# Kernel optimization log

Hardware: AMD Instinct MI355X
Metric: run time of the kernel (lower is better)

Reference implementation:

```python
import jax, jax.numpy as jnp
import numpy as np

HIDDEN = 2048
NUM_HEADS = 16
NUM_KV_HEADS = 8
HEAD_DIM = 128
EPS = 1e-6
ROPE_THETA = 10000.0
T = 2048
Q_SIZE = NUM_HEADS * HEAD_DIM          # 2048
KV_SIZE = NUM_KV_HEADS * HEAD_DIM      # 1024


def setup_inputs() -> dict:
    key = jax.random.key(0)
    k1, k2, k3, k4, k5 = jax.random.split(key, 5)
    positions = jnp.arange(T, dtype=jnp.int32)
    hidden_states = jax.random.normal(k1, (T, HIDDEN), dtype=jnp.float32)
    s = 0.02
    qkv_w = jax.random.normal(k2, (Q_SIZE + 2 * KV_SIZE, HIDDEN), dtype=jnp.float32) * s
    o_w = jax.random.normal(k3, (HIDDEN, Q_SIZE), dtype=jnp.float32) * s
    q_norm_w = jnp.ones((HEAD_DIM,), dtype=jnp.float32) + 0.1 * jax.random.normal(k4, (HEAD_DIM,), dtype=jnp.float32)
    k_norm_w = jnp.ones((HEAD_DIM,), dtype=jnp.float32) + 0.1 * jax.random.normal(k5, (HEAD_DIM,), dtype=jnp.float32)
    return {"positions": positions, "hidden_states": hidden_states,
            "qkv_w": qkv_w, "q_norm_w": q_norm_w, "k_norm_w": k_norm_w, "o_w": o_w}


def _rms_norm(x, w):
    # x: [T, H, D], normalize over last dim
    var = jnp.mean(x * x, axis=-1, keepdims=True)
    return x * jax.lax.rsqrt(var + EPS) * w


def _rope(x, positions):
    # neox-style rotary over full head_dim; x: [T, H, D]
    half = HEAD_DIM // 2
    inv_freq = 1.0 / (ROPE_THETA ** (jnp.arange(0, half, dtype=jnp.float32) / half))
    freqs = positions.astype(jnp.float32)[:, None] * inv_freq  # [T, D/2]
    cos = jnp.cos(freqs)[:, None, :]  # [T, 1, D/2]
    sin = jnp.sin(freqs)[:, None, :]
    x1, x2 = x[..., :half], x[..., half:]
    return jnp.concatenate([x1 * cos - x2 * sin, x2 * cos + x1 * sin], axis=-1)


def reference(positions, hidden_states, qkv_w, q_norm_w, k_norm_w, o_w):
    G = NUM_HEADS // NUM_KV_HEADS  # query groups per kv head
    scale = HEAD_DIM ** -0.5
    qkv = hidden_states @ qkv_w.T  # [T, Q+2KV]
    q, k, v = jnp.split(qkv, [Q_SIZE, Q_SIZE + KV_SIZE], axis=-1)
    q = q.reshape(T, NUM_HEADS, HEAD_DIM)
    k = k.reshape(T, NUM_KV_HEADS, HEAD_DIM)
    v = v.reshape(T, NUM_KV_HEADS, HEAD_DIM)
    # qkv_bias=False path -> per-head RMSNorm on q and k
    q = _rms_norm(q, q_norm_w)
    k = _rms_norm(k, k_norm_w)
    q = _rope(q, positions)
    k = _rope(k, positions)
    # GQA causal attention
    qg = q.reshape(T, NUM_KV_HEADS, G, HEAD_DIM)
    scores = jnp.einsum('qkgd,skd->kgqs', qg, k) * scale  # [KV, G, T, T]
    causal = positions[:, None] >= positions[None, :]  # [T, T]
    scores = jnp.where(causal, scores, jnp.finfo(scores.dtype).min)
    probs = jax.nn.softmax(scores, axis=-1)
    ctx = jnp.einsum('kgqs,skd->qkgd', probs, v)  # [T, KV, G, D]
    ctx = ctx.reshape(T, Q_SIZE)
    return ctx @ o_w.T  # [T, HIDDEN]
```

## Files before the change

### kernel.cpp

```cpp
#include <hip/hip_runtime.h>
#include <math.h>

#define T_SEQ     2048
#define HIDDEN_   2048
#define NUM_HEADS 16
#define NUM_KV    8
#define HEAD_DIM  128
#define Q_SIZE    2048
#define KV_SIZE   1024
#define QKV_N     4096
#define QK_N      3072
#define EPS_      1e-6f

typedef __attribute__((ext_vector_type(8))) short short8;
typedef __attribute__((ext_vector_type(4))) float floatx4;

__device__ __forceinline__ unsigned short f2bf(float f) {
    unsigned int u = __float_as_uint(f);
    u += 0x7fffu + ((u >> 16) & 1u);
    return (unsigned short)(u >> 16);
}
__device__ __forceinline__ float b2f(unsigned short u) {
    return __uint_as_float((unsigned int)u << 16);
}

__device__ __forceinline__ void stage16(const unsigned short* g, unsigned short* lds_base) {
    __builtin_amdgcn_global_load_lds(
        (const __attribute__((address_space(1))) unsigned int*)g,
        (__attribute__((address_space(3))) unsigned int*)lds_base, 16, 0, 0);
}

#define H4 (T_SEQ * HIDDEN_ / 4)
#define W4 (QKV_N * HIDDEN_ / 4)
#define O4 (Q_SIZE * HIDDEN_ / 4)

__global__ __launch_bounds__(256) void convert_all(
    const float* __restrict__ hidden, const float* __restrict__ qkv_w,
    const float* __restrict__ o_w, unsigned short* __restrict__ hbf,
    unsigned short* __restrict__ wbf, unsigned short* __restrict__ obf)
{
    int i = blockIdx.x * 256 + threadIdx.x;
    const float4* src;
    ushort4* dst;
    int j;
    if (i < H4)            { src = (const float4*)hidden; dst = (ushort4*)hbf; j = i; }
    else if (i < H4 + W4)  { src = (const float4*)qkv_w;  dst = (ushort4*)wbf; j = i - H4; }
    else                   { src = (const float4*)o_w;    dst = (ushort4*)obf; j = i - H4 - W4;
                             if (j >= O4) return; }
    float4 v = src[j];
    ushort4 o;
    o.x = f2bf(v.x); o.y = f2bf(v.y); o.z = f2bf(v.z); o.w = f2bf(v.w);
    dst[j] = o;
}

template<int MODE>
__global__ __launch_bounds__(256) void gemm_nt_bf16(
    const unsigned short* __restrict__ A, const unsigned short* __restrict__ B,
    float* __restrict__ C,
    unsigned short* __restrict__ Qb, unsigned short* __restrict__ Kb,
    unsigned short* __restrict__ Vt,
    const int* __restrict__ positions,
    const float* __restrict__ qw, const float* __restrict__ kw,
    int M, int N, int K)
{
    __shared__ unsigned short smem[32768];
    unsigned short* const As0 = smem;
    unsigned short* const Bs0 = smem + 16384;

    const int tid  = threadIdx.x;
    const int w    = tid >> 6;
    const int lane = tid & 63;
    const int colL = lane & 15;
    const int quad = lane >> 4;
    const int bm = blockIdx.y * 128;
    const int bn = blockIdx.x * 128;
    const int wm = (w & 1) * 64;
    const int wn = (w >> 1) * 64;

    floatx4 acc[4][4];
    #pragma unroll
    for (int i = 0; i < 4; ++i)
        #pragma unroll
        for (int j = 0; j < 4; ++j)
            acc[i][j] = (floatx4){0.f, 0.f, 0.f, 0.f};

    int s_r[4], s_lc[4];
    #pragma unroll
    for (int cc = 0; cc < 4; ++cc) {
        int s = cc * 256 + tid;
        int r = s >> 3, pc = s & 7;
        s_r[cc] = r;
        s_lc[cc] = pc ^ (r & 7);
    }

    auto stage_tile = [&](int buf, int k0) {
        unsigned short* la = As0 + buf * 8192;
        unsigned short* lb = Bs0 + buf * 8192;
        #pragma unroll
        for (int cc = 0; cc < 4; ++cc) {
            stage16(A + (size_t)(bm + s_r[cc]) * K + k0 + s_lc[cc] * 8,
                    la + (cc * 256 + w * 64) * 8);
            stage16(B + (size_t)(bn + s_r[cc]) * K + k0 + s_lc[cc] * 8,
                    lb + (cc * 256 + w * 64) * 8);
        }
    };

    const int nt = K >> 6;
    stage_tile(0, 0);

    for (int t = 0; t < nt; ++t) {
        const int b = t & 1;
        if (t + 1 < nt) {
            stage_tile(b ^ 1, (t + 1) << 6);
            asm volatile("s_waitcnt vmcnt(8)" ::: "memory");
        } else {
            asm volatile("s_waitcnt vmcnt(0)" ::: "memory");
        }
        __builtin_amdgcn_s_barrier();
        __builtin_amdgcn_sched_barrier(0);

        const unsigned short* la = As0 + b * 8192;
        const unsigned short* lb = Bs0 + b * 8192;
        #pragma unroll
        for (int kk = 0; kk < 2; ++kk) {
            short8 af[4], bfv[4];
            #pragma unroll
            for (int i = 0; i < 4; ++i) {
                int ra = wm + i * 16 + colL;
                af[i]  = *(const short8*)&la[ra * 64 + (((kk * 4 + quad) ^ (ra & 7)) * 8)];
                int rb = wn + i * 16 + colL;
                bfv[i] = *(const short8*)&lb[rb * 64 + (((kk * 4 + quad) ^ (rb & 7)) * 8)];
            }
            #pragma unroll
            for (int i = 0; i < 4; ++i)
                #pragma unroll
                for (int j = 0; j < 4; ++j)
                    acc[i][j] = __builtin_amdgcn_mfma_f32_16x16x32_bf16(af[i], bfv[j], acc[i][j], 0, 0, 0);
        }
        __builtin_amdgcn_sched_barrier(0);
        asm volatile("" ::: "memory");
        __builtin_amdgcn_s_barrier();
    }

    if constexpr (MODE == 0) {
        #pragma unroll
        for (int i = 0; i < 4; ++i)
            #pragma unroll
            for (int j = 0; j < 4; ++j)
                #pragma unroll
                for (int rr = 0; rr < 4; ++rr) {
                    int row = bm + wm + i * 16 + quad * 4 + rr;
                    int cc2 = bn + wn + j * 16 + colL;
                    C[(size_t)row * N + cc2] = acc[i][j][rr];
                }
    } else {
        if (bn < QK_N) {
            __shared__ float sums[2][128];
            unsigned short* xnL = smem;

            float p[4][4];
            #pragma unroll
            for (int i = 0; i < 4; ++i)
                #pragma unroll
                for (int rr = 0; rr < 4; ++rr) {
                    float s = 0.f;
                    #pragma unroll
                    for (int j = 0; j < 4; ++j)
                        s = fmaf(acc[i][j][rr], acc[i][j][rr], s);
                    p[i][rr] = s;
                }
            #pragma unroll
            for (int off = 1; off < 16; off <<= 1)
                #pragma unroll
                for (int i = 0; i < 4; ++i)
                    #pragma unroll
                    for (int rr = 0; rr < 4; ++rr)
                        p[i][rr] += __shfl_xor(p[i][rr], off, 64);
            if (colL == 0) {
                #pragma unroll
                for (int i = 0; i < 4; ++i)
                    #pragma unroll
                    for (int rr = 0; rr < 4; ++rr)
                        sums[wn >> 6][wm + i * 16 + quad * 4 + rr] = p[i][rr];
            }
            __syncthreads();

            float inv_r[4][4];
            #pragma unroll
            for (int i = 0; i < 4; ++i)
                #pragma unroll
                for (int rr = 0; rr < 4; ++rr) {
                    int row = wm + i * 16 + quad * 4 + rr;
                    float tot = sums[0][row] + sums[1][row];
                    inv_r[i][rr] = rsqrtf(tot * (1.0f / HEAD_DIM) + EPS_);
                }

            const float* nw = (bn < Q_SIZE) ? qw : kw;
            float wv[4];
            #pragma unroll
            for (int j = 0; j < 4; ++j)
                wv[j] = nw[wn + j * 16 + colL];

            #pragma unroll
            for (int i = 0; i < 4; ++i)
                #pragma unroll
                for (int j = 0; j < 4; ++j) {
                    ushort4 pk;
                    pk.x = f2bf(acc[i][j][0] * inv_r[i][0] * wv[j]);
                    pk.y = f2bf(acc[i][j][1] * inv_r[i][1] * wv[j]);
                    pk.z = f2bf(acc[i][j][2] * inv_r[i][2] * wv[j]);
                    pk.w = f2bf(acc[i][j][3] * inv_r[i][3] * wv[j]);
                    int d = wn + j * 16 + colL;
                    *(ushort4*)&xnL[d * 132 + wm + i * 16 + quad * 4] = pk;
                }
            __syncthreads();
            {
                const int r = tid >> 1;
                const int ph = tid & 1;
                const float pos = (float)positions[bm + r];
                const bool is_q = (bn < Q_SIZE);
                const float l2r = 13.287712379549449f / 64.0f;
                const float sc = 0.08838834764831845f;
                unsigned short* rowp;
                if (is_q) rowp = Qb + (size_t)(bm + r) * Q_SIZE + (bn >> 7) * HEAD_DIM;
                else      rowp = Kb + ((size_t)((bn - Q_SIZE) >> 7) * T_SEQ + bm + r) * HEAD_DIM;

                #pragma unroll
                for (int f4 = 0; f4 < 32; f4 += 4) {
                    ushort4 lo, hi;
                    #pragma unroll
                    for (int e = 0; e < 4; ++e) {
                        int f = ph * 32 + f4 + e;
                        float x1 = b2f(xnL[f * 132 + r]);
                        float x2 = b2f(xnL[(f + 64) * 132 + r]);
                        float s, c;
                        __sincosf(pos * exp2f(-(float)f * l2r), &s, &c);
                        float olo = fmaf(x1, c, -x2 * s);
                        float ohi = fmaf(x2, c,  x1 * s);
                        if (is_q) { olo *= sc; ohi *= sc; }
                        ((unsigned short*)&lo)[e] = f2bf(olo);
                        ((unsigned short*)&hi)[e] = f2bf(ohi);
                    }
                    *(ushort4*)(rowp + ph * 32 + f4)      = lo;
                    *(ushort4*)(rowp + 64 + ph * 32 + f4) = hi;
                }
            }
        } else {
            const int kvh = (bn - QK_N) >> 7;
            #pragma unroll
            for (int i = 0; i < 4; ++i)
                #pragma unroll
                for (int j = 0; j < 4; ++j) {
                    int d = wn + j * 16 + colL;
                    int tok = bm + wm + i * 16 + quad * 4;
                    ushort4 o;
                    o.x = f2bf(acc[i][j][0]); o.y = f2bf(acc[i][j][1]);
                    o.z = f2bf(acc[i][j][2]); o.w = f2bf(acc[i][j][3]);
                    *(ushort4*)&Vt[((size_t)kvh * HEAD_DIM + d) * T_SEQ + tok] = o;
                }
        }
    }
}

#define BQ 64
#define BK 64

__global__ __launch_bounds__(256) void attn_mfma(
    const unsigned short* __restrict__ Qb, const unsigned short* __restrict__ Kb,
    const unsigned short* __restrict__ Vt, unsigned short* __restrict__ ctxb,
    float* __restrict__ partO, float* __restrict__ partL)
{
    const int h = blockIdx.y;
    int qt, ch;
    {
        int x = blockIdx.x;
        if (x < 16) { qt = 16 + x; ch = 0; }
        else {
            int p = (x - 16) >> 1;
            if (((x - 16) & 1) == 0) { qt = 15 - p; ch = 0; }
            else                     { qt = 31 - p; ch = 1; }
        }
    }
    const int nch = (qt >= 16) ? 2 : 1;
    const int units = (ch == 0) ? ((qt + 1 < 16) ? qt + 1 : 16) : (qt + 1 - 16);
    const int q0 = qt * BQ;
    const int kv = h >> 1;
    const int tid = threadIdx.x;
    const int w = tid >> 6;
    const int lane = tid & 63;
    const int col = lane & 15;
    const int quad = lane >> 4;

    __shared__ unsigned short Ks[2][64 * 128];
    __shared__ unsigned short Vs[2][144 * 64];
    __shared__ unsigned short Ps[4][16][72];

    {
        int x = tid * 4;
        unsigned short vv = (x < 64) ? (unsigned short)0x3F80 : (unsigned short)0;
        ushort4 o = {vv, vv, vv, vv};
        *(ushort4*)&Vs[0][128 * 64 + x] = o;
        *(ushort4*)&Vs[1][128 * 64 + x] = o;
    }

    short8 qf[4];
    {
        const unsigned short* qp = Qb + (size_t)(q0 + w * 16 + col) * Q_SIZE + h * HEAD_DIM;
        #pragma unroll
        for (int c = 0; c < 4; ++c)
            qf[c] = *(const short8*)(qp + c * 32 + quad * 8);
    }

    const unsigned short* kg[4];
    const unsigned short* vg[4];
    #pragma unroll
    for (int it = 0; it < 4; ++it) {
        int s = it * 256 + tid;
        int kr = s >> 4, kp = s & 15, kj = kp ^ (kr & 15);
        kg[it] = Kb + (size_t)kv * T_SEQ * HEAD_DIM + kr * HEAD_DIM + kj * 8;
        int vr = s >> 3, vp = s & 7, vj = vp ^ (vr & 7);
        vg[it] = Vt + (size_t)kv * HEAD_DIM * T_SEQ + (size_t)vr * T_SEQ + vj * 8;
    }

    floatx4 Ob[9];
    #pragma unroll
    for (int cb = 0; cb < 9; ++cb) Ob[cb] = (floatx4){0.f, 0.f, 0.f, 0.f};

    const int wave_qmin = q0 + w * 16;
    const int wave_qmax = wave_qmin + 15;
    const int tok_base = ch * 1024;

    #pragma unroll
    for (int it = 0; it < 4; ++it) {
        stage16(kg[it] + (size_t)tok_base * HEAD_DIM, &Ks[0][(it * 256 + w * 64) * 8]);
        stage16(vg[it] + tok_base, &Vs[0][(it * 256 + w * 64) * 8]);
    }

    for (int u = 0; u < units; ++u) {
        const int t0 = tok_base + u * BK;
        __syncthreads();
        if (u + 1 < units) {
            const int tn = t0 + BK;
            const int b = (u + 1) & 1;
            #pragma unroll
            for (int it = 0; it < 4; ++it) {
                stage16(kg[it] + (size_t)tn * HEAD_DIM, &Ks[b][(it * 256 + w * 64) * 8]);
                stage16(vg[it] + tn, &Vs[b][(it * 256 + w * 64) * 8]);
            }
        }
        if (t0 > wave_qmax) continue;
        const unsigned short* ks = Ks[u & 1];
        const unsigned short* vs = Vs[u & 1];

        floatx4 S[4];
        #pragma unroll
        for (int cb = 0; cb < 4; ++cb) {
            floatx4 a = (floatx4){0.f, 0.f, 0.f, 0.f};
            #pragma unroll
            for (int c = 0; c < 4; ++c) {
                short8 kf = *(const short8*)&ks[((cb * 16 + col) * 16 + ((c * 4 + quad) ^ col)) * 8];
                a = __builtin_amdgcn_mfma_f32_16x16x32_bf16(kf, qf[c], a, 0, 0, 0);
            }
            S[cb] = a;
        }

        const int qr = q0 + w * 16 + col;
        if (t0 + 63 <= wave_qmin) {
            #pragma unroll
            for (int cb = 0; cb < 4; ++cb) {
                ushort4 pk;
                pk.x = f2bf(__expf(S[cb][0])); pk.y = f2bf(__expf(S[cb][1]));
                pk.z = f2bf(__expf(S[cb][2])); pk.w = f2bf(__expf(S[cb][3]));
                *(ushort4*)&Ps[w][col][cb * 16 + quad * 4] = pk;
            }
        } else {
            #pragma unroll
            for (int cb = 0; cb < 4; ++cb) {
                int kt = t0 + cb * 16 + quad * 4;
                ushort4 pk;
                pk.x = (kt + 0 <= qr) ? f2bf(__expf(S[cb][0])) : (unsigned short)0;
                pk.y = (kt + 1 <= qr) ? f2bf(__expf(S[cb][1])) : (unsigned short)0;
                pk.z = (kt + 2 <= qr) ? f2bf(__expf(S[cb][2])) : (unsigned short)0;
                pk.w = (kt + 3 <= qr) ? f2bf(__expf(S[cb][3])) : (unsigned short)0;
                *(ushort4*)&Ps[w][col][cb * 16 + quad * 4] = pk;
            }
        }

        short8 pf[2];
        pf[0] = *(const short8*)&Ps[w][col][quad * 8];
        pf[1] = *(const short8*)&Ps[w][col][32 + quad * 8];
        #pragma unroll
        for (int cb = 0; cb < 9; ++cb) {
            int vrow = cb * 16 + col;
            #pragma unroll
            for (int kk = 0; kk < 2; ++kk) {
                short8 vf = *(const short8*)&vs[(vrow * 8 + ((kk * 4 + quad) ^ (vrow & 7))) * 8];
                Ob[cb] = __builtin_amdgcn_mfma_f32_16x16x32_bf16(pf[kk], vf, Ob[cb], 0, 0, 0);
            }
        }
    }

    if (nch == 1) {
        #pragma unroll
        for (int r = 0; r < 4; ++r) {
            float l = __shfl(Ob[8][r], lane & 48);
            float rl = 1.0f / l;
            const int qrow = q0 + w * 16 + quad * 4 + r;
            #pragma unroll
            for (int cb = 0; cb < 8; ++cb)
                ctxb[(size_t)qrow * Q_SIZE + h * HEAD_DIM + cb * 16 + col] = f2bf(Ob[cb][r] * rl);
        }
    } else {
        const int slot = (h * 16 + (qt - 16)) * 2 + ch;
        float* po = partO + (size_t)slot * (BQ * HEAD_DIM);
        #pragma unroll
        for (int cb = 0; cb < 8; ++cb)
            #pragma unroll
            for (int r = 0; r < 4; ++r)
                po[(w * 16 + quad * 4 + r) * HEAD_DIM + cb * 16 + col] = Ob[cb][r];
        if (col == 0) {
            #pragma unroll
            for (int r = 0; r < 4; ++r)
                partL[slot * BQ + w * 16 + quad * 4 + r] = Ob[8][r];
        }
    }
}

__global__ __launch_bounds__(256) void combine(
    const float* __restrict__ partO, const float* __restrict__ partL,
    unsigned short* __restrict__ ctxb)
{
    const int h = blockIdx.x >> 4;
    const int qi = blockIdx.x & 15;
    const int q0 = (16 + qi) * 64;
    const int slot0 = (h * 16 + qi) * 2;
    const int tid = threadIdx.x;
    const int row = tid >> 2;
    const int seg = tid & 3;

    const float l = partL[slot0 * 64 + row] + partL[(slot0 + 1) * 64 + row];
    const float rl = 1.0f / l;
    const float* p0 = partO + (size_t)slot0 * 8192 + row * 128 + seg * 32;
    const float* p1 = p0 + 8192;
    unsigned short* dst = ctxb + (size_t)(q0 + row) * Q_SIZE + h * HEAD_DIM + seg * 32;
    #pragma unroll
    for (int m = 0; m < 8; ++m) {
        float4 a = *(const float4*)(p0 + m * 4);
        float4 b = *(const float4*)(p1 + m * 4);
        ushort4 o;
        o.x = f2bf((a.x + b.x) * rl); o.y = f2bf((a.y + b.y) * rl);
        o.z = f2bf((a.z + b.z) * rl); o.w = f2bf((a.w + b.w) * rl);
        *(ushort4*)(dst + m * 4) = o;
    }
}

extern "C" void kernel_launch(void* const* d_in, const int* in_sizes, int n_in,
                              void* d_out, int out_size, void* d_ws, size_t ws_size,
                              hipStream_t stream)
{
    const int*   positions = (const int*)d_in[0];
    const float* hidden    = (const float*)d_in[1];
    const float* qkv_w     = (const float*)d_in[2];
    const float* q_norm_w  = (const float*)d_in[3];
    const float* k_norm_w  = (const float*)d_in[4];
    const float* o_w       = (const float*)d_in[5];
    float* out = (float*)d_out;

    const size_t MB = 1024 * 1024;
    char* ws = (char*)d_ws;
    unsigned short* obf  = (unsigned short*)ws;
    unsigned short* hbf  = (unsigned short*)(ws + 8 * MB);
    unsigned short* wbf  = (unsigned short*)(ws + 16 * MB);
    unsigned short* Vt   = (unsigned short*)(ws + 32 * MB);
    unsigned short* Qb   = (unsigned short*)(ws + 36 * MB);
    unsigned short* Kb   = (unsigned short*)(ws + 44 * MB);
    unsigned short* ctxb = (unsigned short*)(ws + 48 * MB);
    float* partL         = (float*)(ws + 8 * MB);
    float* partO         = (float*)(ws + 16 * MB);

    convert_all<<<(H4 + W4 + O4 + 255) / 256, 256, 0, stream>>>(
        hidden, qkv_w, o_w, hbf, wbf, obf);
    gemm_nt_bf16<1><<<dim3(QKV_N / 128, T_SEQ / 128), 256, 0, stream>>>(
        hbf, wbf, nullptr, Qb, Kb, Vt, positions, q_norm_w, k_norm_w,
        T_SEQ, QKV_N, HIDDEN_);
    attn_mfma<<<dim3(48, NUM_HEADS), 256, 0, stream>>>(Qb, Kb, Vt, ctxb, partO, partL);
    combine<<<256, 256, 0, stream>>>(partO, partL, ctxb);
    gemm_nt_bf16<0><<<dim3(Q_SIZE / 128, T_SEQ / 128), 256, 0, stream>>>(
        ctxb, obf, out, nullptr, nullptr, nullptr, nullptr, nullptr, nullptr,
        T_SEQ, Q_SIZE, HIDDEN_);
}
```

Baseline: 242.1 us.

## Process both GQA query heads per block to share K/V tiles

```diff
diff --git a/kernel.cpp b/kernel.cpp
--- a/kernel.cpp
+++ b/kernel.cpp
@@ -270,7 +270,7 @@
     const unsigned short* __restrict__ Vt, unsigned short* __restrict__ ctxb,
     float* __restrict__ partO, float* __restrict__ partL)
 {
-    const int h = blockIdx.y;
+    const int kv = blockIdx.y;
     int qt, ch;
     {
         int x = blockIdx.x;
@@ -284,7 +284,6 @@
     const int nch = (qt >= 16) ? 2 : 1;
     const int units = (ch == 0) ? ((qt + 1 < 16) ? qt + 1 : 16) : (qt + 1 - 16);
     const int q0 = qt * BQ;
-    const int kv = h >> 1;
     const int tid = threadIdx.x;
     const int w = tid >> 6;
     const int lane = tid & 63;
@@ -303,12 +302,14 @@
         *(ushort4*)&Vs[1][128 * 64 + x] = o;
     }
 
-    short8 qf[4];
-    {
-        const unsigned short* qp = Qb + (size_t)(q0 + w * 16 + col) * Q_SIZE + h * HEAD_DIM;
+    short8 qf[2][4];
+    #pragma unroll
+    for (int g = 0; g < 2; ++g) {
+        const unsigned short* qp = Qb + (size_t)(q0 + w * 16 + col) * Q_SIZE
+                                 + (kv * 2 + g) * HEAD_DIM;
         #pragma unroll
         for (int c = 0; c < 4; ++c)
-            qf[c] = *(const short8*)(qp + c * 32 + quad * 8);
+            qf[g][c] = *(const short8*)(qp + c * 32 + quad * 8);
     }
 
     const unsigned short* kg[4];
@@ -322,9 +323,11 @@
         vg[it] = Vt + (size_t)kv * HEAD_DIM * T_SEQ + (size_t)vr * T_SEQ + vj * 8;
     }
 
-    floatx4 Ob[9];
-    #pragma unroll
-    for (int cb = 0; cb < 9; ++cb) Ob[cb] = (floatx4){0.f, 0.f, 0.f, 0.f};
+    floatx4 Ob[2][9];
+    #pragma unroll
+    for (int g = 0; g < 2; ++g)
+        #pragma unroll
+        for (int cb = 0; cb < 9; ++cb) Ob[g][cb] = (floatx4){0.f, 0.f, 0.f, 0.f};
 
     const int wave_qmin = q0 + w * 16;
     const int wave_qmax = wave_qmin + 15;
@@ -352,76 +355,90 @@
         const unsigned short* ks = Ks[u & 1];
         const unsigned short* vs = Vs[u & 1];
 
-        floatx4 S[4];
+        floatx4 S[2][4];
         #pragma unroll
         for (int cb = 0; cb < 4; ++cb) {
-            floatx4 a = (floatx4){0.f, 0.f, 0.f, 0.f};
+            floatx4 a0 = (floatx4){0.f, 0.f, 0.f, 0.f};
+            floatx4 a1 = (floatx4){0.f, 0.f, 0.f, 0.f};
             #pragma unroll
             for (int c = 0; c < 4; ++c) {
                 short8 kf = *(const short8*)&ks[((cb * 16 + col) * 16 + ((c * 4 + quad) ^ col)) * 8];
-                a = __builtin_amdgcn_mfma_f32_16x16x32_bf16(kf, qf[c], a, 0, 0, 0);
-            }
-            S[cb] = a;
+                a0 = __builtin_amdgcn_mfma_f32_16x16x32_bf16(kf, qf[0][c], a0, 0, 0, 0);
+                a1 = __builtin_amdgcn_mfma_f32_16x16x32_bf16(kf, qf[1][c], a1, 0, 0, 0);
+            }
+            S[0][cb] = a0; S[1][cb] = a1;
         }
 
         const int qr = q0 + w * 16 + col;
-        if (t0 + 63 <= wave_qmin) {
-            #pragma unroll
-            for (int cb = 0; cb < 4; ++cb) {
-                ushort4 pk;
-                pk.x = f2bf(__expf(S[cb][0])); pk.y = f2bf(__expf(S[cb][1]));
-                pk.z = f2bf(__expf(S[cb][2])); pk.w = f2bf(__expf(S[cb][3]));
-                *(ushort4*)&Ps[w][col][cb * 16 + quad * 4] = pk;
-            }
-        } else {
-            #pragma unroll
-            for (int cb = 0; cb < 4; ++cb) {
-                int kt = t0 + cb * 16 + quad * 4;
-                ushort4 pk;
-                pk.x = (kt + 0 <= qr) ? f2bf(__expf(S[cb][0])) : (unsigned short)0;
-                pk.y = (kt + 1 <= qr) ? f2bf(__expf(S[cb][1])) : (unsigned short)0;
-                pk.z = (kt + 2 <= qr) ? f2bf(__expf(S[cb][2])) : (unsigned short)0;
-                pk.w = (kt + 3 <= qr) ? f2bf(__expf(S[cb][3])) : (unsigned short)0;
-                *(ushort4*)&Ps[w][col][cb * 16 + quad * 4] = pk;
-            }
-        }
-
-        short8 pf[2];
-        pf[0] = *(const short8*)&Ps[w][col][quad * 8];
-        pf[1] = *(const short8*)&Ps[w][col][32 + quad * 8];
+        short8 pf[2][2];
+        #pragma unroll
+        for (int g = 0; g < 2; ++g) {
+            if (t0 + 63 <= wave_qmin) {
+                #pragma unroll
+                for (int cb = 0; cb < 4; ++cb) {
+                    ushort4 pk;
+                    pk.x = f2bf(__expf(S[g][cb][0])); pk.y = f2bf(__expf(S[g][cb][1]));
+                    pk.z = f2bf(__expf(S[g][cb][2])); pk.w = f2bf(__expf(S[g][cb][3]));
+                    *(ushort4*)&Ps[w][col][cb * 16 + quad * 4] = pk;
+                }
+            } else {
+                #pragma unroll
+                for (int cb = 0; cb < 4; ++cb) {
+                    int kt = t0 + cb * 16 + quad * 4;
+                    ushort4 pk;
+                    pk.x = (kt + 0 <= qr) ? f2bf(__expf(S[g][cb][0])) : (unsigned short)0;
+                    pk.y = (kt + 1 <= qr) ? f2bf(__expf(S[g][cb][1])) : (unsigned short)0;
+                    pk.z = (kt + 2 <= qr) ? f2bf(__expf(S[g][cb][2])) : (unsigned short)0;
+                    pk.w = (kt + 3 <= qr) ? f2bf(__expf(S[g][cb][3])) : (unsigned short)0;
+                    *(ushort4*)&Ps[w][col][cb * 16 + quad * 4] = pk;
+                }
+            }
+            pf[g][0] = *(const short8*)&Ps[w][col][quad * 8];
+            pf[g][1] = *(const short8*)&Ps[w][col][32 + quad * 8];
+        }
+
         #pragma unroll
         for (int cb = 0; cb < 9; ++cb) {
             int vrow = cb * 16 + col;
             #pragma unroll
             for (int kk = 0; kk < 2; ++kk) {
                 short8 vf = *(const short8*)&vs[(vrow * 8 + ((kk * 4 + quad) ^ (vrow & 7))) * 8];
-                Ob[cb] = __builtin_amdgcn_mfma_f32_16x16x32_bf16(pf[kk], vf, Ob[cb], 0, 0, 0);
+                Ob[0][cb] = __builtin_amdgcn_mfma_f32_16x16x32_bf16(pf[0][kk], vf, Ob[0][cb], 0, 0, 0);
+                Ob[1][cb] = __builtin_amdgcn_mfma_f32_16x16x32_bf16(pf[1][kk], vf, Ob[1][cb], 0, 0, 0);
             }
         }
     }
 
     if (nch == 1) {
         #pragma unroll
-        for (int r = 0; r < 4; ++r) {
-            float l = __shfl(Ob[8][r], lane & 48);
-            float rl = 1.0f / l;
-            const int qrow = q0 + w * 16 + quad * 4 + r;
+        for (int g = 0; g < 2; ++g) {
+            const int h = kv * 2 + g;
+            #pragma unroll
+            for (int r = 0; r < 4; ++r) {
+                float l = __shfl(Ob[g][8][r], lane & 48);
+                float rl = 1.0f / l;
+                const int qrow = q0 + w * 16 + quad * 4 + r;
+                #pragma unroll
+                for (int cb = 0; cb < 8; ++cb)
+                    ctxb[(size_t)qrow * Q_SIZE + h * HEAD_DIM + cb * 16 + col] = f2bf(Ob[g][cb][r] * rl);
+            }
+        }
+    } else {
+        #pragma unroll
+        for (int g = 0; g < 2; ++g) {
+            const int h = kv * 2 + g;
+            const int slot = (h * 16 + (qt - 16)) * 2 + ch;
+            float* po = partO + (size_t)slot * (BQ * HEAD_DIM);
             #pragma unroll
             for (int cb = 0; cb < 8; ++cb)
-                ctxb[(size_t)qrow * Q_SIZE + h * HEAD_DIM + cb * 16 + col] = f2bf(Ob[cb][r] * rl);
-        }
-    } else {
-        const int slot = (h * 16 + (qt - 16)) * 2 + ch;
-        float* po = partO + (size_t)slot * (BQ * HEAD_DIM);
-        #pragma unroll
-        for (int cb = 0; cb < 8; ++cb)
-            #pragma unroll
-            for (int r = 0; r < 4; ++r)
-                po[(w * 16 + quad * 4 + r) * HEAD_DIM + cb * 16 + col] = Ob[cb][r];
-        if (col == 0) {
-            #pragma unroll
-            for (int r = 0; r < 4; ++r)
-                partL[slot * BQ + w * 16 + quad * 4 + r] = Ob[8][r];
+                #pragma unroll
+                for (int r = 0; r < 4; ++r)
+                    po[(w * 16 + quad * 4 + r) * HEAD_DIM + cb * 16 + col] = Ob[g][cb][r];
+            if (col == 0) {
+                #pragma unroll
+                for (int r = 0; r < 4; ++r)
+                    partL[slot * BQ + w * 16 + quad * 4 + r] = Ob[g][8][r];
+            }
         }
     }
 }
@@ -483,7 +500,7 @@
     gemm_nt_bf16<1><<<dim3(QKV_N / 128, T_SEQ / 128), 256, 0, stream>>>(
         hbf, wbf, nullptr, Qb, Kb, Vt, positions, q_norm_w, k_norm_w,
         T_SEQ, QKV_N, HIDDEN_);
-    attn_mfma<<<dim3(48, NUM_HEADS), 256, 0, stream>>>(Qb, Kb, Vt, ctxb, partO, partL);
+    attn_mfma<<<dim3(48, NUM_KV), 256, 0, stream>>>(Qb, Kb, Vt, ctxb, partO, partL);
     combine<<<256, 256, 0, stream>>>(partO, partL, ctxb);
     gemm_nt_bf16<0><<<dim3(Q_SIZE / 128, T_SEQ / 128), 256, 0, stream>>>(
         ctxb, obf, out, nullptr, nullptr, nullptr, nullptr, nullptr, nullptr,
```

After: 257.0 us. 1.06x slower.
